# Kernel optimization log

Hardware: AMD Instinct MI355X
Metric: run time of the kernel (lower is better)

## Reference

```python
import jax, jax.numpy as jnp
import numpy as np

N_V = 40000
N_E = 640000
D_V = 128


def setup_inputs() -> dict:
    key = jax.random.key(0)
    k1, k2, k3, k4 = jax.random.split(key, 4)
    nodes = jax.random.normal(k1, (N_V, D_V), dtype=jnp.float32)
    edge_index = jax.random.randint(k2, (2, N_E), 0, N_V, dtype=jnp.int64)
    # Linear(d_v, d_v) parameters (torch default init: U(-1/sqrt(fan_in), 1/sqrt(fan_in)))
    bound = 1.0 / np.sqrt(D_V)
    W = jax.random.uniform(k3, (D_V, D_V), minval=-bound, maxval=bound, dtype=jnp.float32)
    b = jax.random.uniform(k4, (D_V,), minval=-bound, maxval=bound, dtype=jnp.float32)
    return {"nodes": nodes, "edge_index": edge_index, "W": W, "b": b}


def reference(nodes, edge_index, W, b):
    # GCN: out = act(Linear(D @ (A + I) @ D @ x)), A[src, dst] = 1,
    # deg_j = in-degree of node j (incl. self-loop), d = deg**-0.5.
    # Sparse form: (D A D x)_i = d_i * (sum_{edges (i->j)} d_j x_j + d_i x_i)
    n = nodes.shape[0]
    src, dst = edge_index[0], edge_index[1]
    deg = jax.ops.segment_sum(jnp.ones_like(dst, dtype=nodes.dtype), dst,
                              num_segments=n) + 1.0  # self-loop
    d = jax.lax.rsqrt(deg)                            # [N]
    msg = nodes[dst] * d[dst, None]                   # [E, D] gather
    agg = jax.ops.segment_sum(msg, src, num_segments=n)  # [N, D] scatter-add
    h = d[:, None] * (agg + d[:, None] * nodes)       # normalized aggregation
    return jax.nn.relu(h @ W.T + b)
```

## Files before the change

kernel.cpp:

```cpp
#include <hip/hip_runtime.h>
#include <hip/hip_fp16.h>

typedef short short8 __attribute__((ext_vector_type(8)));
typedef float floatx4 __attribute__((ext_vector_type(4)));

struct f4 { float x, y, z, w; };
struct u4v { unsigned x, y, z, w; };

#define BINW 10240
#define NB   40960
#define CAP  64

__device__ __forceinline__ short f2bf(float f) {
    unsigned u = __builtin_bit_cast(unsigned, f);
    u += 0x7fffu + ((u >> 16) & 1u);
    return (short)(u >> 16);
}

__global__ __launch_bounds__(1024) void k_hist(const int* __restrict__ src,
                                               const int* __restrict__ dst,
                                               unsigned* __restrict__ hist,
                                               int ne, int nchunk) {
    __shared__ unsigned bins[BINW];
    const int c = blockIdx.x >> 1;
    const int which = blockIdx.x & 1;
    const int* __restrict__ arr = which ? dst : src;
    for (int i = threadIdx.x; i < BINW; i += 1024) bins[i] = 0;
    __syncthreads();
    const int csz = (ne + nchunk - 1) / nchunk;
    const int ebeg = c * csz;
    const int eend = min(ne, ebeg + csz);
    for (int e = ebeg + threadIdx.x; e < eend; e += 1024) {
        const unsigned v = (unsigned)arr[e];
        atomicAdd(&bins[v >> 2], 1u << (8 * (v & 3)));
    }
    __syncthreads();
    unsigned* hp = hist + ((size_t)which * nchunk + c) * BINW;
    for (int i = threadIdx.x; i < BINW; i += 1024) hp[i] = bins[i];
}

__global__ void k_scan_conv(const unsigned* __restrict__ hist,
                            unsigned char* __restrict__ woff,
                            unsigned char* __restrict__ m8, float* __restrict__ d,
                            const float* __restrict__ nodes,
                            unsigned* __restrict__ nodes_h,
                            const float* __restrict__ W,
                            unsigned short* __restrict__ W_h,
                            int nv, int nconv, int nchunk) {
    const int i = blockIdx.x * blockDim.x + threadIdx.x;
    if (i < nv) {
        const unsigned char* hs = (const unsigned char*)hist;
        const unsigned char* hd = hs + (size_t)nchunk * NB;
        int acc = 0, deg = 0;
#pragma unroll 4
        for (int c = 0; c < nchunk; ++c) {
            woff[(size_t)c * NB + i] = (unsigned char)min(acc, 255);
            acc += hs[(size_t)c * NB + i];
            deg += hd[(size_t)c * NB + i];
        }
        m8[i] = (unsigned char)min(acc, CAP);
        d[i] = rsqrtf(1.0f + (float)deg);
    }
    if (nodes_h != nullptr && i < nconv) {
        const f4 a = ((const f4*)nodes)[(size_t)i * 2];
        const f4 b = ((const f4*)nodes)[(size_t)i * 2 + 1];
        u4v p;
        p.x = (unsigned)__half_as_ushort(__float2half(a.x)) |
              ((unsigned)__half_as_ushort(__float2half(a.y)) << 16);
        p.y = (unsigned)__half_as_ushort(__float2half(a.z)) |
              ((unsigned)__half_as_ushort(__float2half(a.w)) << 16);
        p.z = (unsigned)__half_as_ushort(__float2half(b.x)) |
              ((unsigned)__half_as_ushort(__float2half(b.y)) << 16);
        p.w = (unsigned)__half_as_ushort(__float2half(b.z)) |
              ((unsigned)__half_as_ushort(__float2half(b.w)) << 16);
        ((u4v*)nodes_h)[i] = p;
    }
    if (i < 2048) {
        const f4 a = ((const f4*)W)[(size_t)i * 2];
        const f4 b = ((const f4*)W)[(size_t)i * 2 + 1];
        u4v p;
        p.x = (unsigned)(unsigned short)f2bf(a.x) | ((unsigned)(unsigned short)f2bf(a.y) << 16);
        p.y = (unsigned)(unsigned short)f2bf(a.z) | ((unsigned)(unsigned short)f2bf(a.w) << 16);
        p.z = (unsigned)(unsigned short)f2bf(b.x) | ((unsigned)(unsigned short)f2bf(b.y) << 16);
        p.w = (unsigned)(unsigned short)f2bf(b.z) | ((unsigned)(unsigned short)f2bf(b.w) << 16);
        ((u4v*)W_h)[i] = p;
    }
}

__global__ __launch_bounds__(1024) void k_fill(const int* __restrict__ src,
                                               const int* __restrict__ dst,
                                               const unsigned char* __restrict__ woff,
                                               unsigned short* __restrict__ adj,
                                               int ne, int nchunk) {
    __shared__ unsigned cur[BINW];
    const int c = blockIdx.x;
    for (int i = threadIdx.x; i < BINW; i += 1024) cur[i] = 0;
    __syncthreads();
    const int csz = (ne + nchunk - 1) / nchunk;
    const int ebeg = c * csz;
    const int eend = min(ne, ebeg + csz);
    const unsigned char* wp = woff + (size_t)c * NB;
    for (int e = ebeg + threadIdx.x; e < eend; e += 1024) {
        const unsigned s = (unsigned)src[e];
        const unsigned sh = 8 * (s & 3);
        const unsigned old = atomicAdd(&cur[s >> 2], 1u << sh);
        const int pos = (int)wp[s] + (int)((old >> sh) & 0xffu);
        if (pos < CAP) adj[(size_t)s * CAP + pos] = (unsigned short)dst[e];
    }
}

__global__ __launch_bounds__(256) void k_gather_gemm(
    const float* __restrict__ nodes, const unsigned* __restrict__ nodes_h,
    const unsigned short* __restrict__ adj, const unsigned char* __restrict__ m8,
    const float* __restrict__ d, const unsigned short* __restrict__ W_h,
    const float* __restrict__ bias, float* __restrict__ out, int nv) {
    __shared__ unsigned short htile[16][136];

    const int wave = threadIdx.x >> 6;
    const int lane = threadIdx.x & 63;
    const int q = lane >> 4;
    const int l16 = lane & 15;
    const int tile = blockIdx.x;

    for (int ii = 0; ii < 4; ++ii) {
        const int node = tile * 16 + wave * 4 + ii;
        int mm = -1, total = 0;
        if (node < nv) { mm = min((int)m8[node], 63); total = mm + 1; }
        const int jl = (lane < mm) ? (int)adj[(size_t)node * CAP + lane]
                                   : ((lane == mm) ? node : 0);
        const float wl = (lane <= mm) ? d[jl] : 0.0f;

        float acc[8];
#pragma unroll
        for (int k = 0; k < 8; ++k) acc[k] = 0.0f;

        if (nodes_h != nullptr) {
            for (int t = 0; t < total; t += 16) {
                const int j0 = __shfl(jl, t + q);
                const float w0 = __shfl(wl, t + q);
                const int j1 = __shfl(jl, t + q + 4);
                const float w1 = __shfl(wl, t + q + 4);
                const int j2 = __shfl(jl, t + q + 8);
                const float w2 = __shfl(wl, t + q + 8);
                const int j3 = __shfl(jl, t + q + 12);
                const float w3 = __shfl(wl, t + q + 12);
                const u4v h0 = ((const u4v*)nodes_h)[(size_t)j0 * 16 + l16];
                const u4v h1 = ((const u4v*)nodes_h)[(size_t)j1 * 16 + l16];
                const u4v h2 = ((const u4v*)nodes_h)[(size_t)j2 * 16 + l16];
                const u4v h3 = ((const u4v*)nodes_h)[(size_t)j3 * 16 + l16];
                const __half2* p0 = (const __half2*)&h0;
                const __half2* p1 = (const __half2*)&h1;
                const __half2* p2 = (const __half2*)&h2;
                const __half2* p3 = (const __half2*)&h3;
#pragma unroll
                for (int k = 0; k < 4; ++k) {
                    float2 f;
                    f = __half22float2(p0[k]); acc[2*k] += w0 * f.x; acc[2*k+1] += w0 * f.y;
                    f = __half22float2(p1[k]); acc[2*k] += w1 * f.x; acc[2*k+1] += w1 * f.y;
                    f = __half22float2(p2[k]); acc[2*k] += w2 * f.x; acc[2*k+1] += w2 * f.y;
                    f = __half22float2(p3[k]); acc[2*k] += w3 * f.x; acc[2*k+1] += w3 * f.y;
                }
            }
        } else {
            for (int t = 0; t < total; t += 4) {
                const int tt = t + q;
                const int j = __shfl(jl, tt);
                const float w = __shfl(wl, tt);
                const f4 v0 = *(const f4*)(nodes + (size_t)j * 128 + l16 * 8);
                const f4 v1 = *(const f4*)(nodes + (size_t)j * 128 + l16 * 8 + 4);
                acc[0] += w * v0.x; acc[1] += w * v0.y; acc[2] += w * v0.z; acc[3] += w * v0.w;
                acc[4] += w * v1.x; acc[5] += w * v1.y; acc[6] += w * v1.z; acc[7] += w * v1.w;
            }
        }

#pragma unroll
        for (int k = 0; k < 8; ++k) {
            acc[k] += __shfl_xor(acc[k], 16);
            acc[k] += __shfl_xor(acc[k], 32);
        }

        if (q == 0) {
            const float di = (node < nv) ? d[node] : 0.0f;
            float hv[8];
#pragma unroll
            for (int k = 0; k < 8; ++k) hv[k] = di * acc[k];
            u4v p;
            p.x = (unsigned)(unsigned short)f2bf(hv[0]) | ((unsigned)(unsigned short)f2bf(hv[1]) << 16);
            p.y = (unsigned)(unsigned short)f2bf(hv[2]) | ((unsigned)(unsigned short)f2bf(hv[3]) << 16);
            p.z = (unsigned)(unsigned short)f2bf(hv[4]) | ((unsigned)(unsigned short)f2bf(hv[5]) << 16);
            p.w = (unsigned)(unsigned short)f2bf(hv[6]) | ((unsigned)(unsigned short)f2bf(hv[7]) << 16);
            *(u4v*)&htile[wave * 4 + ii][l16 * 8] = p;
        }
    }

    __syncthreads();

    const int l15 = lane & 15;
    const int lhi = lane >> 4;

    short8 Af[4];
#pragma unroll
    for (int kt = 0; kt < 4; ++kt)
        Af[kt] = *(const short8*)&htile[l15][kt * 32 + lhi * 8];

#pragma unroll
    for (int n2 = 0; n2 < 2; ++n2) {
        const int nt = wave * 2 + n2;
        const float bv = bias[nt * 16 + l15];
        floatx4 acc = {0.f, 0.f, 0.f, 0.f};
#pragma unroll
        for (int kt = 0; kt < 4; ++kt) {
            const short8 Bf = *(const short8*)(W_h + (size_t)(nt * 16 + l15) * 128 + kt * 32 + lhi * 8);
            acc = __builtin_amdgcn_mfma_f32_16x16x32_bf16(Af[kt], Bf, acc, 0, 0, 0);
        }
#pragma unroll
        for (int r = 0; r < 4; ++r) {
            const int row = tile * 16 + lhi * 4 + r;
            if (row < nv)
                out[(size_t)row * 128 + nt * 16 + l15] = fmaxf(acc[r] + bv, 0.0f);
        }
    }
}

extern "C" void kernel_launch(void* const* d_in, const int* in_sizes, int n_in,
                              void* d_out, int out_size, void* d_ws, size_t ws_size,
                              hipStream_t stream) {
    const float* nodes = (const float*)d_in[0];
    const int*   ei    = (const int*)d_in[1];
    const float* W     = (const float*)d_in[2];
    const float* bias  = (const float*)d_in[3];
    float* out = (float*)d_out;

    const int NV = in_sizes[0] / 128;
    const int NE = in_sizes[1] / 2;
    const int* src = ei;
    const int* dst = ei + NE;

    const size_t words = ws_size / 4;
    auto need = [&](int nchunk, bool fp16) {
        return (size_t)2 * nchunk * BINW + (size_t)nchunk * (NB / 4) +
               (NB / 4) + (size_t)NV + 8192 + (size_t)NV * (CAP / 2) +
               (fp16 ? (size_t)NV * 64 : 0);
    };
    int nchunk = 128; bool use_fp16 = true;
    if (need(nchunk, use_fp16) > words) nchunk = 64;
    if (need(nchunk, use_fp16) > words) nchunk = 32;
    if (need(nchunk, use_fp16) > words) { nchunk = 128; use_fp16 = false; }
    if (need(nchunk, use_fp16) > words) nchunk = 64;
    if (need(nchunk, use_fp16) > words) nchunk = 32;

    int* w = (int*)d_ws;
    unsigned* hist = (unsigned*)w;
    unsigned char* woff = (unsigned char*)(hist + (size_t)2 * nchunk * BINW);
    unsigned char* m8   = woff + (size_t)nchunk * NB;
    float* d = (float*)(m8 + NB);
    unsigned short* W_h = (unsigned short*)(d + NV);
    unsigned short* adj = W_h + 16384;
    unsigned* nodes_h = use_fp16 ? (unsigned*)(adj + (size_t)NV * CAP) : nullptr;

    k_hist<<<nchunk * 2, 1024, 0, stream>>>(src, dst, hist, NE, nchunk);

    const int nconv = NV * 16;
    const int nthreads = max(NV, nconv);
    k_scan_conv<<<(nthreads + 255) / 256, 256, 0, stream>>>(
        hist, woff, m8, d, nodes, nodes_h, W, W_h, NV, nconv, nchunk);

    k_fill<<<nchunk, 1024, 0, stream>>>(src, dst, woff, adj, NE, nchunk);

    const int ntiles = (NV + 15) / 16;
    k_gather_gemm<<<ntiles, 256, 0, stream>>>(nodes, nodes_h, adj, m8, d,
                                              W_h, bias, out, NV);
}
```

Before: 77.64 us.

## Split fused gather+GEMM into column-partitioned gather kernel and separate MFMA GEMM kernel

The fused gather-then-GEMM kernel is split into two kernels. The gather kernel assigns 8 lanes per node and partitions the 128 feature columns across 8 blocks (column groups), so each block streams a narrow slice of the fp16 neighbour rows. It writes a bf16 intermediate h to workspace. The GEMM kernel keeps all of W in registers and processes one 16-row tile per wave. This aims to improve parallelism and cache locality in the gather, at the cost of an extra global round trip for h, one more launch, and narrower 4-byte gathers.

```diff
diff --git a/kernel.cpp b/kernel.cpp
--- a/kernel.cpp
+++ b/kernel.cpp
@@ -5,6 +5,7 @@
 typedef float floatx4 __attribute__((ext_vector_type(4)));
 
 struct f4 { float x, y, z, w; };
+struct f2v { float x, y; };
 struct u4v { unsigned x, y, z, w; };
 
 #define BINW 10240
@@ -109,115 +110,86 @@
     }
 }
 
-__global__ __launch_bounds__(256) void k_gather_gemm(
+__global__ __launch_bounds__(256) void k_gather_cp(
     const float* __restrict__ nodes, const unsigned* __restrict__ nodes_h,
     const unsigned short* __restrict__ adj, const unsigned char* __restrict__ m8,
-    const float* __restrict__ d, const unsigned short* __restrict__ W_h,
-    const float* __restrict__ bias, float* __restrict__ out, int nv) {
-    __shared__ unsigned short htile[16][136];
-
+    const float* __restrict__ d, unsigned* __restrict__ h, int nv) {
+    const int cg = blockIdx.x & 7;
+    const int ntile = blockIdx.x >> 3;
+    const int slot = threadIdx.x >> 3;
+    const int l8 = threadIdx.x & 7;
+    const int wbase = ((threadIdx.x & 63) >> 3) << 3;
+    const int node = ntile * 32 + slot;
+    if (node >= nv) return;
+
+    const int m = min((int)m8[node], 63);
+    const int total = m + 1;
+    const int rounds = (total + 7) >> 3;
+
+    float a0 = 0.0f, a1 = 0.0f;
+    for (int r = 0; r < rounds; ++r) {
+        const int idx = r * 8 + l8;
+        const int jr = (idx < m) ? (int)adj[(size_t)node * CAP + idx] : node;
+        const float wr = (idx <= m) ? d[jr] : 0.0f;
+#pragma unroll
+        for (int t = 0; t < 8; ++t) {
+            const int j = __shfl(jr, wbase + t);
+            const float w = __shfl(wr, wbase + t);
+            if (nodes_h != nullptr) {
+                const unsigned u = nodes_h[(size_t)j * 64 + cg * 8 + l8];
+                const float2 f = __half22float2(__builtin_bit_cast(__half2, u));
+                a0 += w * f.x;
+                a1 += w * f.y;
+            } else {
+                const f2v f = *(const f2v*)(nodes + (size_t)j * 128 + cg * 16 + l8 * 2);
+                a0 += w * f.x;
+                a1 += w * f.y;
+            }
+        }
+    }
+    const float di = d[node];
+    const unsigned p = (unsigned)(unsigned short)f2bf(di * a0) |
+                       ((unsigned)(unsigned short)f2bf(di * a1) << 16);
+    h[(size_t)node * 64 + cg * 8 + l8] = p;
+}
+
+__global__ __launch_bounds__(256) void k_gemm(
+    const unsigned short* __restrict__ h, const unsigned short* __restrict__ W_h,
+    const float* __restrict__ bias, float* __restrict__ out, int ntiles, int nv) {
     const int wave = threadIdx.x >> 6;
     const int lane = threadIdx.x & 63;
-    const int q = lane >> 4;
-    const int l16 = lane & 15;
-    const int tile = blockIdx.x;
-
-    for (int ii = 0; ii < 4; ++ii) {
-        const int node = tile * 16 + wave * 4 + ii;
-        int mm = -1, total = 0;
-        if (node < nv) { mm = min((int)m8[node], 63); total = mm + 1; }
-        const int jl = (lane < mm) ? (int)adj[(size_t)node * CAP + lane]
-                                   : ((lane == mm) ? node : 0);
-        const float wl = (lane <= mm) ? d[jl] : 0.0f;
-
-        float acc[8];
-#pragma unroll
-        for (int k = 0; k < 8; ++k) acc[k] = 0.0f;
-
-        if (nodes_h != nullptr) {
-            for (int t = 0; t < total; t += 16) {
-                const int j0 = __shfl(jl, t + q);
-                const float w0 = __shfl(wl, t + q);
-                const int j1 = __shfl(jl, t + q + 4);
-                const float w1 = __shfl(wl, t + q + 4);
-                const int j2 = __shfl(jl, t + q + 8);
-                const float w2 = __shfl(wl, t + q + 8);
-                const int j3 = __shfl(jl, t + q + 12);
-                const float w3 = __shfl(wl, t + q + 12);
-                const u4v h0 = ((const u4v*)nodes_h)[(size_t)j0 * 16 + l16];
-                const u4v h1 = ((const u4v*)nodes_h)[(size_t)j1 * 16 + l16];
-                const u4v h2 = ((const u4v*)nodes_h)[(size_t)j2 * 16 + l16];
-                const u4v h3 = ((const u4v*)nodes_h)[(size_t)j3 * 16 + l16];
-                const __half2* p0 = (const __half2*)&h0;
-                const __half2* p1 = (const __half2*)&h1;
-                const __half2* p2 = (const __half2*)&h2;
-                const __half2* p3 = (const __half2*)&h3;
-#pragma unroll
-                for (int k = 0; k < 4; ++k) {
-                    float2 f;
-                    f = __half22float2(p0[k]); acc[2*k] += w0 * f.x; acc[2*k+1] += w0 * f.y;
-                    f = __half22float2(p1[k]); acc[2*k] += w1 * f.x; acc[2*k+1] += w1 * f.y;
-                    f = __half22float2(p2[k]); acc[2*k] += w2 * f.x; acc[2*k+1] += w2 * f.y;
-                    f = __half22float2(p3[k]); acc[2*k] += w3 * f.x; acc[2*k+1] += w3 * f.y;
-                }
-            }
-        } else {
-            for (int t = 0; t < total; t += 4) {
-                const int tt = t + q;
-                const int j = __shfl(jl, tt);
-                const float w = __shfl(wl, tt);
-                const f4 v0 = *(const f4*)(nodes + (size_t)j * 128 + l16 * 8);
-                const f4 v1 = *(const f4*)(nodes + (size_t)j * 128 + l16 * 8 + 4);
-                acc[0] += w * v0.x; acc[1] += w * v0.y; acc[2] += w * v0.z; acc[3] += w * v0.w;
-                acc[4] += w * v1.x; acc[5] += w * v1.y; acc[6] += w * v1.z; acc[7] += w * v1.w;
-            }
-        }
-
-#pragma unroll
-        for (int k = 0; k < 8; ++k) {
-            acc[k] += __shfl_xor(acc[k], 16);
-            acc[k] += __shfl_xor(acc[k], 32);
-        }
-
-        if (q == 0) {
-            const float di = (node < nv) ? d[node] : 0.0f;
-            float hv[8];
-#pragma unroll
-            for (int k = 0; k < 8; ++k) hv[k] = di * acc[k];
-            u4v p;
-            p.x = (unsigned)(unsigned short)f2bf(hv[0]) | ((unsigned)(unsigned short)f2bf(hv[1]) << 16);
-            p.y = (unsigned)(unsigned short)f2bf(hv[2]) | ((unsigned)(unsigned short)f2bf(hv[3]) << 16);
-            p.z = (unsigned)(unsigned short)f2bf(hv[4]) | ((unsigned)(unsigned short)f2bf(hv[5]) << 16);
-            p.w = (unsigned)(unsigned short)f2bf(hv[6]) | ((unsigned)(unsigned short)f2bf(hv[7]) << 16);
-            *(u4v*)&htile[wave * 4 + ii][l16 * 8] = p;
-        }
-    }
-
-    __syncthreads();
-
     const int l15 = lane & 15;
     const int lhi = lane >> 4;
 
-    short8 Af[4];
-#pragma unroll
-    for (int kt = 0; kt < 4; ++kt)
-        Af[kt] = *(const short8*)&htile[l15][kt * 32 + lhi * 8];
-
-#pragma unroll
-    for (int n2 = 0; n2 < 2; ++n2) {
-        const int nt = wave * 2 + n2;
-        const float bv = bias[nt * 16 + l15];
-        floatx4 acc = {0.f, 0.f, 0.f, 0.f};
-#pragma unroll
-        for (int kt = 0; kt < 4; ++kt) {
-            const short8 Bf = *(const short8*)(W_h + (size_t)(nt * 16 + l15) * 128 + kt * 32 + lhi * 8);
-            acc = __builtin_amdgcn_mfma_f32_16x16x32_bf16(Af[kt], Bf, acc, 0, 0, 0);
-        }
-#pragma unroll
-        for (int r = 0; r < 4; ++r) {
-            const int row = tile * 16 + lhi * 4 + r;
-            if (row < nv)
-                out[(size_t)row * 128 + nt * 16 + l15] = fmaxf(acc[r] + bv, 0.0f);
+    short8 Bf[8][4];
+#pragma unroll
+    for (int nt = 0; nt < 8; ++nt)
+#pragma unroll
+        for (int kt = 0; kt < 4; ++kt)
+            Bf[nt][kt] = *(const short8*)(W_h + (size_t)(nt * 16 + l15) * 128 + kt * 32 + lhi * 8);
+
+    float bias8[8];
+#pragma unroll
+    for (int nt = 0; nt < 8; ++nt) bias8[nt] = bias[nt * 16 + l15];
+
+    for (int tile = blockIdx.x * 4 + wave; tile < ntiles; tile += gridDim.x * 4) {
+        short8 Af[4];
+#pragma unroll
+        for (int kt = 0; kt < 4; ++kt)
+            Af[kt] = *(const short8*)(h + (size_t)(tile * 16 + l15) * 128 + kt * 32 + lhi * 8);
+
+#pragma unroll
+        for (int nt = 0; nt < 8; ++nt) {
+            floatx4 acc = {0.f, 0.f, 0.f, 0.f};
+#pragma unroll
+            for (int kt = 0; kt < 4; ++kt)
+                acc = __builtin_amdgcn_mfma_f32_16x16x32_bf16(Af[kt], Bf[nt][kt], acc, 0, 0, 0);
+#pragma unroll
+            for (int r = 0; r < 4; ++r) {
+                const int row = tile * 16 + lhi * 4 + r;
+                if (row < nv)
+                    out[(size_t)row * 128 + nt * 16 + l15] = fmaxf(acc[r] + bias8[nt], 0.0f);
+            }
         }
     }
 }
@@ -240,7 +212,7 @@
     auto need = [&](int nchunk, bool fp16) {
         return (size_t)2 * nchunk * BINW + (size_t)nchunk * (NB / 4) +
                (NB / 4) + (size_t)NV + 8192 + (size_t)NV * (CAP / 2) +
-               (fp16 ? (size_t)NV * 64 : 0);
+               (size_t)NV * 64 + (fp16 ? (size_t)NV * 64 : 0);
     };
     int nchunk = 128; bool use_fp16 = true;
     if (need(nchunk, use_fp16) > words) nchunk = 64;
@@ -256,7 +228,8 @@
     float* d = (float*)(m8 + NB);
     unsigned short* W_h = (unsigned short*)(d + NV);
     unsigned short* adj = W_h + 16384;
-    unsigned* nodes_h = use_fp16 ? (unsigned*)(adj + (size_t)NV * CAP) : nullptr;
+    unsigned* h = (unsigned*)(adj + (size_t)NV * CAP);
+    unsigned* nodes_h = use_fp16 ? h + (size_t)NV * 64 : nullptr;
 
     k_hist<<<nchunk * 2, 1024, 0, stream>>>(src, dst, hist, NE, nchunk);
 
@@ -267,7 +240,10 @@
 
     k_fill<<<nchunk, 1024, 0, stream>>>(src, dst, woff, adj, NE, nchunk);
 
+    const int nt32 = (NV + 31) / 32;
+    k_gather_cp<<<nt32 * 8, 256, 0, stream>>>(nodes, nodes_h, adj, m8, d, h, NV);
+
     const int ntiles = (NV + 15) / 16;
-    k_gather_gemm<<<ntiles, 256, 0, stream>>>(nodes, nodes_h, adj, m8, d,
-                                              W_h, bias, out, NV);
-}
+    k_gemm<<<(ntiles + 3) / 4, 256, 0, stream>>>((const unsigned short*)h, W_h,
+                                                 bias, out, ntiles, NV);
+}
```

Measured after the change: 142.9 us. 1.84x slower.

## Build adjacency via two-pass bucketed sort instead of per-node histogram offsets

Applied to the files above, without the earlier changes.

Replaces the per-node source histogram and byte-offset scan with a coarse 128-node bucket count, scatters edges into per-bucket buffers, then builds each bucket's adjacency rows in shared memory and writes them out coalesced. The in-degree histogram now shares a pass with the bucket counting, halving the hist blocks. This is meant to cut the large per-node offset tables and the scattered 2-byte adjacency writes, at the cost of an extra kernel launch and an intermediate edge buffer. Buckets over 4096 edges or nodes over 64 neighbours are truncated, and the workspace layout is now sized from a fixed 40960 nodes.

```diff
diff --git a/kernel.cpp b/kernel.cpp
--- a/kernel.cpp
+++ b/kernel.cpp
@@ -9,6 +9,8 @@
 
 #define BINW 10240
 #define NB   40960
+#define NBKT 320
+#define EBCAP 4096
 #define CAP  64
 
 __device__ __forceinline__ short f2bf(float f) {
@@ -20,28 +22,34 @@
 __global__ __launch_bounds__(1024) void k_hist(const int* __restrict__ src,
                                                const int* __restrict__ dst,
                                                unsigned* __restrict__ hist,
+                                               unsigned* __restrict__ cnt_cb,
                                                int ne, int nchunk) {
     __shared__ unsigned bins[BINW];
-    const int c = blockIdx.x >> 1;
-    const int which = blockIdx.x & 1;
-    const int* __restrict__ arr = which ? dst : src;
+    __shared__ unsigned cb[NBKT];
+    const int c = blockIdx.x;
     for (int i = threadIdx.x; i < BINW; i += 1024) bins[i] = 0;
+    for (int i = threadIdx.x; i < NBKT; i += 1024) cb[i] = 0;
     __syncthreads();
     const int csz = (ne + nchunk - 1) / nchunk;
     const int ebeg = c * csz;
     const int eend = min(ne, ebeg + csz);
     for (int e = ebeg + threadIdx.x; e < eend; e += 1024) {
-        const unsigned v = (unsigned)arr[e];
-        atomicAdd(&bins[v >> 2], 1u << (8 * (v & 3)));
-    }
-    __syncthreads();
-    unsigned* hp = hist + ((size_t)which * nchunk + c) * BINW;
+        const unsigned t = (unsigned)dst[e];
+        atomicAdd(&bins[t >> 2], 1u << (8 * (t & 3)));
+        const unsigned s = (unsigned)src[e];
+        atomicAdd(&cb[s >> 7], 1u);
+    }
+    __syncthreads();
+    unsigned* hp = hist + (size_t)c * BINW;
     for (int i = threadIdx.x; i < BINW; i += 1024) hp[i] = bins[i];
+    unsigned* cp = cnt_cb + (size_t)c * NBKT;
+    for (int i = threadIdx.x; i < NBKT; i += 1024) cp[i] = cb[i];
 }
 
 __global__ void k_scan_conv(const unsigned* __restrict__ hist,
-                            unsigned char* __restrict__ woff,
-                            unsigned char* __restrict__ m8, float* __restrict__ d,
+                            const unsigned* __restrict__ cnt_cb,
+                            unsigned* __restrict__ cb_off, unsigned* __restrict__ btot,
+                            float* __restrict__ d,
                             const float* __restrict__ nodes,
                             unsigned* __restrict__ nodes_h,
                             const float* __restrict__ W,
@@ -49,17 +57,20 @@
                             int nv, int nconv, int nchunk) {
     const int i = blockIdx.x * blockDim.x + threadIdx.x;
     if (i < nv) {
-        const unsigned char* hs = (const unsigned char*)hist;
-        const unsigned char* hd = hs + (size_t)nchunk * NB;
-        int acc = 0, deg = 0;
+        const unsigned char* hd = (const unsigned char*)hist;
+        int deg = 0;
 #pragma unroll 4
+        for (int c = 0; c < nchunk; ++c) deg += hd[(size_t)c * NB + i];
+        d[i] = rsqrtf(1.0f + (float)deg);
+    }
+    if (i < NBKT) {
+        const int b = i;
+        unsigned acc = 0;
         for (int c = 0; c < nchunk; ++c) {
-            woff[(size_t)c * NB + i] = (unsigned char)min(acc, 255);
-            acc += hs[(size_t)c * NB + i];
-            deg += hd[(size_t)c * NB + i];
-        }
-        m8[i] = (unsigned char)min(acc, CAP);
-        d[i] = rsqrtf(1.0f + (float)deg);
+            cb_off[(size_t)c * NBKT + b] = acc;
+            acc += cnt_cb[(size_t)c * NBKT + b];
+        }
+        btot[b] = acc;
     }
     if (nodes_h != nullptr && i < nconv) {
         const f4 a = ((const f4*)nodes)[(size_t)i * 2];
@@ -87,26 +98,51 @@
     }
 }
 
-__global__ __launch_bounds__(1024) void k_fill(const int* __restrict__ src,
-                                               const int* __restrict__ dst,
-                                               const unsigned char* __restrict__ woff,
-                                               unsigned short* __restrict__ adj,
-                                               int ne, int nchunk) {
-    __shared__ unsigned cur[BINW];
+__global__ __launch_bounds__(1024) void k_fill_p1(const int* __restrict__ src,
+                                                  const int* __restrict__ dst,
+                                                  const unsigned* __restrict__ cb_off,
+                                                  unsigned* __restrict__ ebuf,
+                                                  int ne, int nchunk) {
+    __shared__ unsigned cur[NBKT];
     const int c = blockIdx.x;
-    for (int i = threadIdx.x; i < BINW; i += 1024) cur[i] = 0;
+    for (int i = threadIdx.x; i < NBKT; i += 1024) cur[i] = 0;
     __syncthreads();
     const int csz = (ne + nchunk - 1) / nchunk;
     const int ebeg = c * csz;
     const int eend = min(ne, ebeg + csz);
-    const unsigned char* wp = woff + (size_t)c * NB;
+    const unsigned* co = cb_off + (size_t)c * NBKT;
     for (int e = ebeg + threadIdx.x; e < eend; e += 1024) {
         const unsigned s = (unsigned)src[e];
-        const unsigned sh = 8 * (s & 3);
-        const unsigned old = atomicAdd(&cur[s >> 2], 1u << sh);
-        const int pos = (int)wp[s] + (int)((old >> sh) & 0xffu);
-        if (pos < CAP) adj[(size_t)s * CAP + pos] = (unsigned short)dst[e];
-    }
+        const unsigned b = s >> 7;
+        const unsigned pos = co[b] + atomicAdd(&cur[b], 1u);
+        if (pos < EBCAP)
+            ebuf[(size_t)b * EBCAP + pos] = ((s & 127u) << 16) | (unsigned)dst[e];
+    }
+}
+
+__global__ __launch_bounds__(1024) void k_fill_p2(const unsigned* __restrict__ ebuf,
+                                                  const unsigned* __restrict__ btot,
+                                                  unsigned short* __restrict__ adj,
+                                                  unsigned char* __restrict__ m8) {
+    __shared__ unsigned short a[128][CAP];
+    __shared__ unsigned cur[128];
+    const int b = blockIdx.x;
+    for (int i = threadIdx.x; i < 128; i += 1024) cur[i] = 0;
+    __syncthreads();
+    const unsigned tot = min(btot[b], (unsigned)EBCAP);
+    const unsigned* ep = ebuf + (size_t)b * EBCAP;
+    for (unsigned k = threadIdx.x; k < tot; k += 1024) {
+        const unsigned u = ep[k];
+        const unsigned sl = u >> 16;
+        const unsigned pos = atomicAdd(&cur[sl], 1u);
+        if (pos < CAP) a[sl][pos] = (unsigned short)(u & 0xffffu);
+    }
+    __syncthreads();
+    unsigned* ao = (unsigned*)(adj + (size_t)b * 128 * CAP);
+    const unsigned* as = (const unsigned*)a;
+    for (int i = threadIdx.x; i < 128 * CAP / 2; i += 1024) ao[i] = as[i];
+    if (threadIdx.x < 128)
+        m8[b * 128 + threadIdx.x] = (unsigned char)min(cur[threadIdx.x], (unsigned)CAP);
 }
 
 __global__ __launch_bounds__(256) void k_gather_gemm(
@@ -238,9 +274,10 @@
 
     const size_t words = ws_size / 4;
     auto need = [&](int nchunk, bool fp16) {
-        return (size_t)2 * nchunk * BINW + (size_t)nchunk * (NB / 4) +
-               (NB / 4) + (size_t)NV + 8192 + (size_t)NV * (CAP / 2) +
-               (fp16 ? (size_t)NV * 64 : 0);
+        return (size_t)nchunk * BINW + (size_t)2 * nchunk * NBKT + NBKT +
+               (size_t)NB + 8192 + (size_t)NB * (CAP / 2) + (NB / 4) +
+               (size_t)NBKT * EBCAP + (size_t)NB * 64 +
+               (fp16 ? (size_t)NB * 64 : 0);
     };
     int nchunk = 128; bool use_fp16 = true;
     if (need(nchunk, use_fp16) > words) nchunk = 64;
@@ -249,23 +286,29 @@
     if (need(nchunk, use_fp16) > words) nchunk = 64;
     if (need(nchunk, use_fp16) > words) nchunk = 32;
 
-    int* w = (int*)d_ws;
-    unsigned* hist = (unsigned*)w;
-    unsigned char* woff = (unsigned char*)(hist + (size_t)2 * nchunk * BINW);
-    unsigned char* m8   = woff + (size_t)nchunk * NB;
-    float* d = (float*)(m8 + NB);
-    unsigned short* W_h = (unsigned short*)(d + NV);
-    unsigned short* adj = W_h + 16384;
-    unsigned* nodes_h = use_fp16 ? (unsigned*)(adj + (size_t)NV * CAP) : nullptr;
-
-    k_hist<<<nchunk * 2, 1024, 0, stream>>>(src, dst, hist, NE, nchunk);
+    unsigned* p = (unsigned*)d_ws;
+    unsigned* hist   = p;                       p += (size_t)nchunk * BINW;
+    unsigned* cnt_cb = p;                       p += (size_t)nchunk * NBKT;
+    unsigned* cb_off = p;                       p += (size_t)nchunk * NBKT;
+    unsigned* btot   = p;                       p += NBKT;
+    float*    d      = (float*)p;               p += NB;
+    unsigned short* W_h = (unsigned short*)p;   p += 8192;
+    unsigned short* adj = (unsigned short*)p;   p += (size_t)NB * (CAP / 2);
+    unsigned char* m8 = (unsigned char*)p;      p += NB / 4;
+    unsigned* ebuf   = p;                       p += (size_t)NBKT * EBCAP;
+    unsigned* h      = p;                       p += (size_t)NB * 64;
+    unsigned* nodes_h = use_fp16 ? p : nullptr;
+    (void)h;
+
+    k_hist<<<nchunk, 1024, 0, stream>>>(src, dst, hist, cnt_cb, NE, nchunk);
 
     const int nconv = NV * 16;
     const int nthreads = max(NV, nconv);
     k_scan_conv<<<(nthreads + 255) / 256, 256, 0, stream>>>(
-        hist, woff, m8, d, nodes, nodes_h, W, W_h, NV, nconv, nchunk);
-
-    k_fill<<<nchunk, 1024, 0, stream>>>(src, dst, woff, adj, NE, nchunk);
+        hist, cnt_cb, cb_off, btot, d, nodes, nodes_h, W, W_h, NV, nconv, nchunk);
+
+    k_fill_p1<<<nchunk, 1024, 0, stream>>>(src, dst, cb_off, ebuf, NE, nchunk);
+    k_fill_p2<<<NBKT, 1024, 0, stream>>>(ebuf, btot, adj, m8);
 
     const int ntiles = (NV + 15) / 16;
     k_gather_gemm<<<ntiles, 256, 0, stream>>>(nodes, nodes_h, adj, m8, d,
```

Result: slower. 101.6 us (+30.8%).

## Fuse fp16/bf16 conversion into histogram pass and tile the chunk scan through LDS

Applied to the files above, without the earlier changes.

Moves the node fp16 and W bf16 conversions into the histogram kernel as a grid-stride loop, so they run alongside the edge histogramming. The scan becomes its own kernel that stages 128 chunk rows per 256-node tile in shared memory and writes offsets back with coalesced word stores, replacing strided byte accesses. The dst histogram now uses 32 chunks instead of 128, cutting its size and the work of the degree reduction. The workspace layout is fixed and there is no fallback to fewer chunks, so a smaller workspace would only disable fp16.

```diff
diff --git a/kernel.cpp b/kernel.cpp
--- a/kernel.cpp
+++ b/kernel.cpp
@@ -10,6 +10,8 @@
 #define BINW 10240
 #define NB   40960
 #define CAP  64
+#define NCHS 128
+#define NCHD 32
 
 __device__ __forceinline__ short f2bf(float f) {
     unsigned u = __builtin_bit_cast(unsigned, f);
@@ -19,15 +21,21 @@
 
 __global__ __launch_bounds__(1024) void k_hist(const int* __restrict__ src,
                                                const int* __restrict__ dst,
-                                               unsigned* __restrict__ hist,
-                                               int ne, int nchunk) {
+                                               unsigned* __restrict__ hsrc,
+                                               unsigned* __restrict__ hdst,
+                                               const float* __restrict__ nodes,
+                                               unsigned* __restrict__ nodes_h,
+                                               const float* __restrict__ W,
+                                               unsigned short* __restrict__ W_h,
+                                               int ne, int nconv) {
     __shared__ unsigned bins[BINW];
-    const int c = blockIdx.x >> 1;
-    const int which = blockIdx.x & 1;
-    const int* __restrict__ arr = which ? dst : src;
+    const bool is_src = blockIdx.x < NCHS;
+    const int c = is_src ? blockIdx.x : blockIdx.x - NCHS;
+    const int nch = is_src ? NCHS : NCHD;
+    const int* __restrict__ arr = is_src ? src : dst;
     for (int i = threadIdx.x; i < BINW; i += 1024) bins[i] = 0;
     __syncthreads();
-    const int csz = (ne + nchunk - 1) / nchunk;
+    const int csz = (ne + nch - 1) / nch;
     const int ebeg = c * csz;
     const int eend = min(ne, ebeg + csz);
     for (int e = ebeg + threadIdx.x; e < eend; e += 1024) {
@@ -35,71 +43,88 @@
         atomicAdd(&bins[v >> 2], 1u << (8 * (v & 3)));
     }
     __syncthreads();
-    unsigned* hp = hist + ((size_t)which * nchunk + c) * BINW;
+    unsigned* hp = (is_src ? hsrc : hdst) + (size_t)c * BINW;
     for (int i = threadIdx.x; i < BINW; i += 1024) hp[i] = bins[i];
-}
-
-__global__ void k_scan_conv(const unsigned* __restrict__ hist,
-                            unsigned char* __restrict__ woff,
-                            unsigned char* __restrict__ m8, float* __restrict__ d,
-                            const float* __restrict__ nodes,
-                            unsigned* __restrict__ nodes_h,
-                            const float* __restrict__ W,
-                            unsigned short* __restrict__ W_h,
-                            int nv, int nconv, int nchunk) {
-    const int i = blockIdx.x * blockDim.x + threadIdx.x;
-    if (i < nv) {
-        const unsigned char* hs = (const unsigned char*)hist;
-        const unsigned char* hd = hs + (size_t)nchunk * NB;
-        int acc = 0, deg = 0;
-#pragma unroll 4
-        for (int c = 0; c < nchunk; ++c) {
-            woff[(size_t)c * NB + i] = (unsigned char)min(acc, 255);
-            acc += hs[(size_t)c * NB + i];
-            deg += hd[(size_t)c * NB + i];
-        }
-        m8[i] = (unsigned char)min(acc, CAP);
-        d[i] = rsqrtf(1.0f + (float)deg);
-    }
-    if (nodes_h != nullptr && i < nconv) {
-        const f4 a = ((const f4*)nodes)[(size_t)i * 2];
-        const f4 b = ((const f4*)nodes)[(size_t)i * 2 + 1];
-        u4v p;
-        p.x = (unsigned)__half_as_ushort(__float2half(a.x)) |
-              ((unsigned)__half_as_ushort(__float2half(a.y)) << 16);
-        p.y = (unsigned)__half_as_ushort(__float2half(a.z)) |
-              ((unsigned)__half_as_ushort(__float2half(a.w)) << 16);
-        p.z = (unsigned)__half_as_ushort(__float2half(b.x)) |
-              ((unsigned)__half_as_ushort(__float2half(b.y)) << 16);
-        p.w = (unsigned)__half_as_ushort(__float2half(b.z)) |
-              ((unsigned)__half_as_ushort(__float2half(b.w)) << 16);
-        ((u4v*)nodes_h)[i] = p;
-    }
-    if (i < 2048) {
-        const f4 a = ((const f4*)W)[(size_t)i * 2];
-        const f4 b = ((const f4*)W)[(size_t)i * 2 + 1];
+
+    const int gi = blockIdx.x * 1024 + threadIdx.x;
+    if (nodes_h != nullptr) {
+        for (int i = gi; i < nconv; i += (NCHS + NCHD) * 1024) {
+            const f4 a = ((const f4*)nodes)[(size_t)i * 2];
+            const f4 b = ((const f4*)nodes)[(size_t)i * 2 + 1];
+            u4v p;
+            p.x = (unsigned)__half_as_ushort(__float2half(a.x)) |
+                  ((unsigned)__half_as_ushort(__float2half(a.y)) << 16);
+            p.y = (unsigned)__half_as_ushort(__float2half(a.z)) |
+                  ((unsigned)__half_as_ushort(__float2half(a.w)) << 16);
+            p.z = (unsigned)__half_as_ushort(__float2half(b.x)) |
+                  ((unsigned)__half_as_ushort(__float2half(b.y)) << 16);
+            p.w = (unsigned)__half_as_ushort(__float2half(b.z)) |
+                  ((unsigned)__half_as_ushort(__float2half(b.w)) << 16);
+            ((u4v*)nodes_h)[i] = p;
+        }
+    }
+    if (gi < 2048) {
+        const f4 a = ((const f4*)W)[(size_t)gi * 2];
+        const f4 b = ((const f4*)W)[(size_t)gi * 2 + 1];
         u4v p;
         p.x = (unsigned)(unsigned short)f2bf(a.x) | ((unsigned)(unsigned short)f2bf(a.y) << 16);
         p.y = (unsigned)(unsigned short)f2bf(a.z) | ((unsigned)(unsigned short)f2bf(a.w) << 16);
         p.z = (unsigned)(unsigned short)f2bf(b.x) | ((unsigned)(unsigned short)f2bf(b.y) << 16);
         p.w = (unsigned)(unsigned short)f2bf(b.z) | ((unsigned)(unsigned short)f2bf(b.w) << 16);
-        ((u4v*)W_h)[i] = p;
+        ((u4v*)W_h)[gi] = p;
+    }
+}
+
+__global__ __launch_bounds__(256) void k_scan(const unsigned* __restrict__ hsrc,
+                                              const unsigned* __restrict__ hdst,
+                                              unsigned* __restrict__ woff,
+                                              unsigned char* __restrict__ m8,
+                                              float* __restrict__ d, int nv) {
+    __shared__ unsigned char T[NCHS][256];
+    const int base = blockIdx.x * 256;
+    const int wbase = base >> 2;
+    unsigned* Tw = (unsigned*)T;
+    for (int idx = threadIdx.x; idx < NCHS * 64; idx += 256) {
+        const int c = idx >> 6, w = idx & 63;
+        Tw[c * 64 + w] = hsrc[(size_t)c * BINW + wbase + w];
+    }
+    __syncthreads();
+    const int i = base + threadIdx.x;
+    int acc = 0;
+#pragma unroll 4
+    for (int c = 0; c < NCHS; ++c) {
+        const int v = T[c][threadIdx.x];
+        T[c][threadIdx.x] = (unsigned char)min(acc, 255);
+        acc += v;
+    }
+    m8[i] = (unsigned char)min(acc, CAP);
+    {
+        const unsigned char* hd = (const unsigned char*)hdst;
+        int deg = 0;
+#pragma unroll
+        for (int c = 0; c < NCHD; ++c) deg += hd[(size_t)c * NB + i];
+        d[i] = rsqrtf(1.0f + (float)deg);
+    }
+    __syncthreads();
+    for (int idx = threadIdx.x; idx < NCHS * 64; idx += 256) {
+        const int c = idx >> 6, w = idx & 63;
+        woff[(size_t)c * BINW + wbase + w] = Tw[c * 64 + w];
     }
 }
 
 __global__ __launch_bounds__(1024) void k_fill(const int* __restrict__ src,
                                                const int* __restrict__ dst,
-                                               const unsigned char* __restrict__ woff,
+                                               const unsigned* __restrict__ woff,
                                                unsigned short* __restrict__ adj,
-                                               int ne, int nchunk) {
+                                               int ne) {
     __shared__ unsigned cur[BINW];
     const int c = blockIdx.x;
     for (int i = threadIdx.x; i < BINW; i += 1024) cur[i] = 0;
     __syncthreads();
-    const int csz = (ne + nchunk - 1) / nchunk;
+    const int csz = (ne + NCHS - 1) / NCHS;
     const int ebeg = c * csz;
     const int eend = min(ne, ebeg + csz);
-    const unsigned char* wp = woff + (size_t)c * NB;
+    const unsigned char* wp = (const unsigned char*)(woff + (size_t)c * BINW);
     for (int e = ebeg + threadIdx.x; e < eend; e += 1024) {
         const unsigned s = (unsigned)src[e];
         const unsigned sh = 8 * (s & 3);
@@ -237,35 +262,28 @@
     const int* dst = ei + NE;
 
     const size_t words = ws_size / 4;
-    auto need = [&](int nchunk, bool fp16) {
-        return (size_t)2 * nchunk * BINW + (size_t)nchunk * (NB / 4) +
-               (NB / 4) + (size_t)NV + 8192 + (size_t)NV * (CAP / 2) +
-               (fp16 ? (size_t)NV * 64 : 0);
-    };
-    int nchunk = 128; bool use_fp16 = true;
-    if (need(nchunk, use_fp16) > words) nchunk = 64;
-    if (need(nchunk, use_fp16) > words) nchunk = 32;
-    if (need(nchunk, use_fp16) > words) { nchunk = 128; use_fp16 = false; }
-    if (need(nchunk, use_fp16) > words) nchunk = 64;
-    if (need(nchunk, use_fp16) > words) nchunk = 32;
-
-    int* w = (int*)d_ws;
-    unsigned* hist = (unsigned*)w;
-    unsigned char* woff = (unsigned char*)(hist + (size_t)2 * nchunk * BINW);
-    unsigned char* m8   = woff + (size_t)nchunk * NB;
-    float* d = (float*)(m8 + NB);
-    unsigned short* W_h = (unsigned short*)(d + NV);
-    unsigned short* adj = W_h + 16384;
-    unsigned* nodes_h = use_fp16 ? (unsigned*)(adj + (size_t)NV * CAP) : nullptr;
-
-    k_hist<<<nchunk * 2, 1024, 0, stream>>>(src, dst, hist, NE, nchunk);
+    const size_t base_w = (size_t)NCHS * BINW + (size_t)NCHD * BINW +
+                          (size_t)NCHS * BINW + (NB / 4) + (size_t)NB + 8192 +
+                          (size_t)NB * (CAP / 2);
+    const bool use_fp16 = (base_w + (size_t)NB * 64) <= words;
+
+    unsigned* p = (unsigned*)d_ws;
+    unsigned* hsrc = p;                         p += (size_t)NCHS * BINW;
+    unsigned* hdst = p;                         p += (size_t)NCHD * BINW;
+    unsigned* woff = p;                         p += (size_t)NCHS * BINW;
+    unsigned char* m8 = (unsigned char*)p;      p += NB / 4;
+    float* d = (float*)p;                       p += NB;
+    unsigned short* W_h = (unsigned short*)p;   p += 8192;
+    unsigned short* adj = (unsigned short*)p;   p += (size_t)NB * (CAP / 2);
+    unsigned* nodes_h = use_fp16 ? p : nullptr;
 
     const int nconv = NV * 16;
-    const int nthreads = max(NV, nconv);
-    k_scan_conv<<<(nthreads + 255) / 256, 256, 0, stream>>>(
-        hist, woff, m8, d, nodes, nodes_h, W, W_h, NV, nconv, nchunk);
-
-    k_fill<<<nchunk, 1024, 0, stream>>>(src, dst, woff, adj, NE, nchunk);
+    k_hist<<<NCHS + NCHD, 1024, 0, stream>>>(src, dst, hsrc, hdst,
+                                             nodes, nodes_h, W, W_h, NE, nconv);
+
+    k_scan<<<NB / 256, 256, 0, stream>>>(hsrc, hdst, woff, m8, d, NV);
+
+    k_fill<<<NCHS, 1024, 0, stream>>>(src, dst, woff, adj, NE);
 
     const int ntiles = (NV + 15) / 16;
     k_gather_gemm<<<ntiles, 256, 0, stream>>>(nodes, nodes_h, adj, m8, d,
```

After: 74.93 us. 3.5% less time.
